# Kernel tuning notes

Hardware: AMD Instinct MI355X
Metric: run time of the kernel (lower is better)

The kernel has to match this reference:

```python
import jax, jax.numpy as jnp
import numpy as np

B, C, H, W = 8, 64, 512, 512
NUM_S = 256
EPS = 1e-7

# 3x3 neighborhood offsets excluding the center (row-major order, matching
# torch.cat([f[:, :, :4], f[:, :, 5:]], 2) after flatten of the 3x3 patch)
_DH = jnp.array([0, 0, 0, 1, 1, 2, 2, 2])
_DW = jnp.array([0, 1, 2, 0, 2, 0, 1, 2])


def setup_inputs() -> dict:
    key = jax.random.key(0)
    k1, k2, k3 = jax.random.split(key, 3)
    feat_q = jax.random.normal(k1, (B, C, H, W), dtype=jnp.float32)
    feat_k = jax.random.normal(k2, (B, C, H, W), dtype=jnp.float32)
    # h_id, w_id in [0, H-3] inclusive -> randint upper bound H-2 = 510
    sample_ids = jax.random.randint(k3, (NUM_S, 2), 0, H - 2)
    return {"feat_q": feat_q, "feat_k": feat_k, "sample_ids": sample_ids}


def _neighbor_sample(feat, sample_ids):
    # feat: [b, c, h, w]; sample_ids: [num_s, 2]
    b, c, h, w = feat.shape
    hi = sample_ids[:, 0]
    wi = sample_ids[:, 1]
    # gather 8 neighbors per sampled location: [b, c, num_s, 8]
    nb = feat[:, :, hi[:, None] + _DH[None, :], wi[:, None] + _DW[None, :]]
    # center pixel: [b, c, num_s, 1]
    ctr = feat[:, :, hi + 1, wi + 1][:, :, :, None]
    ft = (nb - ctr).reshape(b, c, -1)  # [b, c, 8*num_s]
    # L2 normalize over channel dim (Normalize(power=2) with eps=1e-7)
    norm = jnp.sqrt(jnp.sum(ft * ft, axis=1, keepdims=True))
    return ft / (norm + EPS)


def reference(feat_q, feat_k, sample_ids):
    f_q = _neighbor_sample(feat_q, sample_ids)
    f_k = _neighbor_sample(feat_k, sample_ids)
    # L1Loss with default mean reduction; single layer (num_l=1)
    return jnp.mean(jnp.abs(f_q - f_k))
```

## Files before the change

### kernel.cpp

```cpp
#include <hip/hip_runtime.h>
#include <hip/hip_bf16.h>

#define NUM_SAMPLES 256
#define CH 64
#define IMG_H 512
#define IMG_W 512
#define BATCH 8
#define NBLOCKS (BATCH * NUM_SAMPLES)

__device__ __forceinline__ float wave_reduce_sum(float v) {
    v += __shfl_xor(v, 32, 64);
    v += __shfl_xor(v, 16, 64);
    v += __shfl_xor(v, 8, 64);
    v += __shfl_xor(v, 4, 64);
    v += __shfl_xor(v, 2, 64);
    v += __shfl_xor(v, 1, 64);
    return v;
}

__global__ void __launch_bounds__(128)
sample_diff_kernel(const float* __restrict__ fq,
                   const float* __restrict__ fk,
                   const int* __restrict__ ids,
                   float* __restrict__ partial) {
    const int c   = threadIdx.x & 63;
    const int wid = threadIdx.x >> 6;
    const int bs  = blockIdx.x;
    const int b   = bs >> 8;
    const int s   = bs & (NUM_SAMPLES - 1);

    const int hi = ids[2 * s + 0];
    const int wi = ids[2 * s + 1];

    const float* __restrict__ src = (wid == 0) ? fq : fk;

    const size_t HW   = (size_t)IMG_H * IMG_W;
    const size_t base = ((size_t)(b * CH + c)) * HW + (size_t)hi * IMG_W + wi;

    float pv[9];
#pragma unroll
    for (int r = 0; r < 3; ++r) {
#pragma unroll
        for (int col = 0; col < 3; ++col) {
            pv[r * 3 + col] = src[base + (size_t)r * IMG_W + col];
        }
    }

    const float ctr = pv[4];

    float d[8];
    d[0] = pv[0] - ctr; d[1] = pv[1] - ctr; d[2] = pv[2] - ctr;
    d[3] = pv[3] - ctr; d[4] = pv[5] - ctr; d[5] = pv[6] - ctr;
    d[6] = pv[7] - ctr; d[7] = pv[8] - ctr;

    float nv[8];
#pragma unroll
    for (int n = 0; n < 8; ++n) {
        const float ss = wave_reduce_sum(d[n] * d[n]);
        nv[n] = d[n] * (1.0f / (sqrtf(ss) + 1e-7f));
    }

    __shared__ float kx[8][64];
    if (wid == 1) {
#pragma unroll
        for (int n = 0; n < 8; ++n) kx[n][c] = nv[n];
    }
    __syncthreads();
    if (wid == 0) {
        float acc = 0.0f;
#pragma unroll
        for (int n = 0; n < 8; ++n) acc += fabsf(nv[n] - kx[n][c]);
        acc = wave_reduce_sum(acc);
        if (c == 0) partial[bs] = acc;
    }
}

__global__ void __launch_bounds__(64)
final_reduce_kernel(const float* __restrict__ partial, float* __restrict__ out) {
    const int c = threadIdx.x;
    float v = 0.0f;
#pragma unroll
    for (int i = 0; i < NBLOCKS / 64; ++i)
        v += partial[i * 64 + c];
    v = wave_reduce_sum(v);
    if (c == 0) {
        out[0] = v * (1.0f / 1048576.0f);
    }
}

extern "C" void kernel_launch(void* const* d_in, const int* in_sizes, int n_in,
                              void* d_out, int out_size, void* d_ws, size_t ws_size,
                              hipStream_t stream) {
    const float* fq  = (const float*)d_in[0];
    const float* fk  = (const float*)d_in[1];
    const int*   ids = (const int*)d_in[2];
    float* out     = (float*)d_out;
    float* partial = (float*)d_ws;

    sample_diff_kernel<<<NBLOCKS, 128, 0, stream>>>(fq, fk, ids, partial);
    final_reduce_kernel<<<1, 64, 0, stream>>>(partial, out);
}
```

Baseline: 29.68 us.

## Split 3x3 patch rows across four waves and widen final reduction

The sample kernel now uses four waves per block: each feature tensor gets two waves, one handling the top two patch rows and one the bottom row, so each wave issues fewer dependent gathers and shuffle reductions. Row loads use pairs of aligned float2 reads with a parity select instead of three scalar loads. The final reduction uses 256 threads with float4 loads in place of a 64-thread serial loop. This adds a second block barrier, shared-memory traffic, and a redundant center load in the bottom-row wave.

```diff
diff --git a/kernel.cpp b/kernel.cpp
--- a/kernel.cpp
+++ b/kernel.cpp
@@ -18,13 +18,26 @@
     return v;
 }
 
-__global__ void __launch_bounds__(128)
+__device__ __forceinline__ void load_trio(const float* __restrict__ src,
+                                          size_t e, float t[3]) {
+    const size_t ea = e & ~(size_t)1;
+    const int o = (int)(e & 1);
+    const float2 A = *(const float2*)(src + ea);
+    const float2 B = *(const float2*)(src + ea + 2);
+    t[0] = o ? A.y : A.x;
+    t[1] = o ? B.x : A.y;
+    t[2] = o ? B.y : B.x;
+}
+
+__global__ void __launch_bounds__(256)
 sample_diff_kernel(const float* __restrict__ fq,
                    const float* __restrict__ fk,
                    const int* __restrict__ ids,
                    float* __restrict__ partial) {
     const int c   = threadIdx.x & 63;
     const int wid = threadIdx.x >> 6;
+    const int rg  = wid & 1;
+    const int tk  = wid >> 1;
     const int bs  = blockIdx.x;
     const int b   = bs >> 8;
     const int s   = bs & (NUM_SAMPLES - 1);
@@ -32,59 +45,76 @@
     const int hi = ids[2 * s + 0];
     const int wi = ids[2 * s + 1];
 
-    const float* __restrict__ src = (wid == 0) ? fq : fk;
+    const float* __restrict__ src = tk ? fk : fq;
+    const size_t chbase = (size_t)(b * CH + c) * ((size_t)IMG_H * IMG_W);
+    const size_t rowoff = (size_t)hi * IMG_W + wi;
 
-    const size_t HW   = (size_t)IMG_H * IMG_W;
-    const size_t base = ((size_t)(b * CH + c)) * HW + (size_t)hi * IMG_W + wi;
+    __shared__ float kx[8][64];
+    __shared__ float sm[2];
 
-    float pv[9];
-#pragma unroll
-    for (int r = 0; r < 3; ++r) {
-#pragma unroll
-        for (int col = 0; col < 3; ++col) {
-            pv[r * 3 + col] = src[base + (size_t)r * IMG_W + col];
+    float nv0, nv1, nv2, nv3, nv4;
+
+    if (rg == 0) {
+        float t0[3], t1[3];
+        load_trio(src, chbase + rowoff, t0);
+        load_trio(src, chbase + rowoff + IMG_W, t1);
+        const float ctr = t1[1];
+        const float d0 = t0[0] - ctr, d1 = t0[1] - ctr, d2 = t0[2] - ctr;
+        const float d3 = t1[0] - ctr, d4 = t1[2] - ctr;
+        nv0 = d0 * (1.0f / (sqrtf(wave_reduce_sum(d0 * d0)) + 1e-7f));
+        nv1 = d1 * (1.0f / (sqrtf(wave_reduce_sum(d1 * d1)) + 1e-7f));
+        nv2 = d2 * (1.0f / (sqrtf(wave_reduce_sum(d2 * d2)) + 1e-7f));
+        nv3 = d3 * (1.0f / (sqrtf(wave_reduce_sum(d3 * d3)) + 1e-7f));
+        nv4 = d4 * (1.0f / (sqrtf(wave_reduce_sum(d4 * d4)) + 1e-7f));
+        if (tk == 1) {
+            kx[0][c] = nv0; kx[1][c] = nv1; kx[2][c] = nv2;
+            kx[3][c] = nv3; kx[4][c] = nv4;
+        }
+    } else {
+        float t2[3];
+        load_trio(src, chbase + rowoff + 2 * IMG_W, t2);
+        const float ctr = src[chbase + rowoff + IMG_W + 1];
+        const float d0 = t2[0] - ctr, d1 = t2[1] - ctr, d2 = t2[2] - ctr;
+        nv0 = d0 * (1.0f / (sqrtf(wave_reduce_sum(d0 * d0)) + 1e-7f));
+        nv1 = d1 * (1.0f / (sqrtf(wave_reduce_sum(d1 * d1)) + 1e-7f));
+        nv2 = d2 * (1.0f / (sqrtf(wave_reduce_sum(d2 * d2)) + 1e-7f));
+        nv3 = 0.0f; nv4 = 0.0f;
+        if (tk == 1) {
+            kx[5][c] = nv0; kx[6][c] = nv1; kx[7][c] = nv2;
         }
     }
+    __syncthreads();
 
-    const float ctr = pv[4];
-
-    float d[8];
-    d[0] = pv[0] - ctr; d[1] = pv[1] - ctr; d[2] = pv[2] - ctr;
-    d[3] = pv[3] - ctr; d[4] = pv[5] - ctr; d[5] = pv[6] - ctr;
-    d[6] = pv[7] - ctr; d[7] = pv[8] - ctr;
-
-    float nv[8];
-#pragma unroll
-    for (int n = 0; n < 8; ++n) {
-        const float ss = wave_reduce_sum(d[n] * d[n]);
-        nv[n] = d[n] * (1.0f / (sqrtf(ss) + 1e-7f));
-    }
-
-    __shared__ float kx[8][64];
-    if (wid == 1) {
-#pragma unroll
-        for (int n = 0; n < 8; ++n) kx[n][c] = nv[n];
+    if (tk == 0) {
+        float acc;
+        if (rg == 0) {
+            acc = fabsf(nv0 - kx[0][c]) + fabsf(nv1 - kx[1][c]) +
+                  fabsf(nv2 - kx[2][c]) + fabsf(nv3 - kx[3][c]) +
+                  fabsf(nv4 - kx[4][c]);
+        } else {
+            acc = fabsf(nv0 - kx[5][c]) + fabsf(nv1 - kx[6][c]) +
+                  fabsf(nv2 - kx[7][c]);
+        }
+        acc = wave_reduce_sum(acc);
+        if (c == 0) sm[rg] = acc;
     }
     __syncthreads();
-    if (wid == 0) {
-        float acc = 0.0f;
-#pragma unroll
-        for (int n = 0; n < 8; ++n) acc += fabsf(nv[n] - kx[n][c]);
-        acc = wave_reduce_sum(acc);
-        if (c == 0) partial[bs] = acc;
-    }
+    if (threadIdx.x == 0) partial[bs] = sm[0] + sm[1];
 }
 
-__global__ void __launch_bounds__(64)
+__global__ void __launch_bounds__(256)
 final_reduce_kernel(const float* __restrict__ partial, float* __restrict__ out) {
-    const int c = threadIdx.x;
-    float v = 0.0f;
-#pragma unroll
-    for (int i = 0; i < NBLOCKS / 64; ++i)
-        v += partial[i * 64 + c];
+    __shared__ float sm[4];
+    const int t = threadIdx.x;
+    const float4 v0 = ((const float4*)partial)[t * 2 + 0];
+    const float4 v1 = ((const float4*)partial)[t * 2 + 1];
+    float v = v0.x + v0.y + v0.z + v0.w + v1.x + v1.y + v1.z + v1.w;
     v = wave_reduce_sum(v);
-    if (c == 0) {
-        out[0] = v * (1.0f / 1048576.0f);
+    if ((t & 63) == 0) sm[t >> 6] = v;
+    __syncthreads();
+    if (t == 0) {
+        const float tot = sm[0] + sm[1] + sm[2] + sm[3];
+        out[0] = tot * (1.0f / 1048576.0f);
     }
 }
 
@@ -97,6 +127,6 @@
     float* out     = (float*)d_out;
     float* partial = (float*)d_ws;
 
-    sample_diff_kernel<<<NBLOCKS, 128, 0, stream>>>(fq, fk, ids, partial);
-    final_reduce_kernel<<<1, 64, 0, stream>>>(partial, out);
+    sample_diff_kernel<<<NBLOCKS, 256, 0, stream>>>(fq, fk, ids, partial);
+    final_reduce_kernel<<<1, 256, 0, stream>>>(partial, out);
 }
```

Measured after the change: 30.28 us. 2.0% more time.
